# Kernel optimization log

Measured on AMD Instinct MI355X. Metric: run time of the kernel, lower is better.

The kernel has to match this reference:

```python
import jax, jax.numpy as jnp
import numpy as np

WIN = 8          # window_size
DIM = 96         # embedding dim
HEADS = 3        # num_heads
N = WIN * WIN    # tokens per window
B_ = 8192        # total windows (2 images * 64*64 windows)
NUM_WIN = 4096   # windows per image (mask leading dim)


def _relative_position_index():
    # Same construction as the torch module (meshgrid default 'ij').
    ch = np.arange(WIN)
    coords = np.stack(np.meshgrid(ch, ch, indexing="ij"))          # [2, W, W]
    flat = coords.reshape(2, -1)                                     # [2, N]
    rel = flat[:, :, None] - flat[:, None, :]                        # [2, N, N]
    rel = rel.transpose(1, 2, 0).astype(np.int32)                    # [N, N, 2]
    rel[:, :, 0] += WIN - 1
    rel[:, :, 1] += WIN - 1
    rel[:, :, 0] *= 2 * WIN - 1
    return rel.sum(-1)                                               # [N, N] int32


def setup_inputs() -> dict:
    key = jax.random.key(0)
    ks = jax.random.split(key, 8)
    x = jax.random.normal(ks[0], (B_, N, DIM), dtype=jnp.float32)
    mask = jax.random.normal(ks[1], (NUM_WIN, N, N), dtype=jnp.float32)
    s = 0.02
    qkv_w = jax.random.normal(ks[2], (3 * DIM, DIM), dtype=jnp.float32) * s
    qkv_b = jax.random.normal(ks[3], (3 * DIM,), dtype=jnp.float32) * s
    proj_w = jax.random.normal(ks[4], (DIM, DIM), dtype=jnp.float32) * s
    proj_b = jax.random.normal(ks[5], (DIM,), dtype=jnp.float32) * s
    n_bias = (2 * WIN - 1) * (2 * WIN - 1)  # 225
    bias_table = jax.random.normal(ks[6], (n_bias, HEADS), dtype=jnp.float32) * s
    rel_idx = jnp.asarray(_relative_position_index())  # [N, N] int32
    return {"x": x, "mask": mask, "qkv_w": qkv_w, "qkv_b": qkv_b,
            "proj_w": proj_w, "proj_b": proj_b, "bias_table": bias_table,
            "rel_idx": rel_idx}


def reference(x, mask, qkv_w, qkv_b, proj_w, proj_b, bias_table, rel_idx):
    Bw, n, C = x.shape
    hd = C // HEADS
    scale = hd ** (-0.5)
    qkv = (x @ qkv_w.T + qkv_b).reshape(Bw, n, 3, HEADS, hd)
    qkv = jnp.transpose(qkv, (2, 0, 3, 1, 4))
    q, k, v = qkv[0], qkv[1], qkv[2]
    attn = jnp.einsum("bhqd,bhkd->bhqk", q * scale, k)              # [Bw, H, n, n]
    # relative position bias gather: [n, n, H] -> [H, n, n]
    bias = bias_table[rel_idx.reshape(-1)].reshape(n, n, HEADS)
    attn = attn + jnp.transpose(bias, (2, 0, 1))[None]
    # shift mask: broadcast over (batch, heads)
    nw = mask.shape[0]
    attn = attn.reshape(Bw // nw, nw, HEADS, n, n) + mask[None, :, None]
    attn = attn.reshape(Bw, HEADS, n, n)
    attn = jax.nn.softmax(attn, axis=-1)
    out = jnp.einsum("bhqk,bhkd->bhqd", attn, v)                    # [Bw, H, n, hd]
    out = jnp.transpose(out, (0, 2, 1, 3)).reshape(Bw, n, C)
    return out @ proj_w.T + proj_b
```

## Files before the change

kernel.cpp:

```cpp
#include <hip/hip_runtime.h>

typedef __attribute__((ext_vector_type(8))) short short8v;
typedef __attribute__((ext_vector_type(4))) float f32x4;

#define INVLN2 1.4426950408889634f

__device__ __forceinline__ ushort f2bf(float f) {
  union { float f; unsigned int u; } c; c.f = f;
  return (ushort)((c.u + 0x7FFFu + ((c.u >> 16) & 1u)) >> 16);
}

__device__ __forceinline__ unsigned cvtpk(float a, float b) {
  unsigned r;
  asm("v_cvt_pk_bf16_f32 %0, %1, %2" : "=v"(r) : "v"(a), "v"(b));
  return r;
}

__device__ __forceinline__ float exp2w(float x) {
#if __has_builtin(__builtin_amdgcn_exp2f)
  return __builtin_amdgcn_exp2f(x);
#else
  return __expf(x * 0.6931471805599453f);
#endif
}

__device__ __forceinline__ short8v bits8(unsigned a, unsigned b, unsigned c, unsigned d) {
  union { unsigned u[4]; short8v s; } cv;
  cv.u[0] = a; cv.u[1] = b; cv.u[2] = c; cv.u[3] = d;
  return cv.s;
}

__global__ __launch_bounds__(256) void setup_k(
    const float* __restrict__ qkv_w, const float* __restrict__ proj_w,
    const float* __restrict__ bias_table, const int* __restrict__ rel_idx,
    const float* __restrict__ qkv_b,
    ushort* __restrict__ qkv_wb, ushort* __restrict__ proj_wb,
    float* __restrict__ bias_comb, float* __restrict__ qkv_bs) {
  const float qs = 0.17677669529663687f * INVLN2;
  int idx = blockIdx.x * 256 + threadIdx.x;
  if (idx < 27648) {
    qkv_wb[idx] = f2bf(qkv_w[idx] * (idx < 9216 ? qs : 1.0f));
  } else if (idx < 36864) {
    int i = idx - 27648;
    int cw = i / 96, j = i % 96;
    int h = j >> 5, kk = j & 31;
    int g = kk >> 3, b = (kk & 4) >> 2, d = kk & 3;
    int src = h * 32 + 16 * b + 4 * g + d;
    proj_wb[i] = f2bf(proj_w[cw * 96 + src]);
  } else if (idx < 49152) {
    int i = idx - 36864;
    int h = i / 4096, rc = i % 4096;
    bias_comb[i] = bias_table[rel_idx[rc] * 3 + h] * INVLN2;
  } else if (idx < 49440) {
    int i = idx - 49152;
    qkv_bs[i] = qkv_b[i] * (i < 96 ? qs : 1.0f);
  }
}

__global__ __launch_bounds__(256, 2) void winattn(
    const float* __restrict__ x, const float* __restrict__ mask,
    const ushort* __restrict__ qkv_wb, const ushort* __restrict__ proj_wb,
    const float* __restrict__ bias_comb, const float* __restrict__ qkv_bs,
    const float* __restrict__ proj_b, float* __restrict__ out) {
  __shared__ ushort klds[2][64][104];
  __shared__ ushort vts[2][96][64];

  const int bb = blockIdx.x;
  const int t = threadIdx.x;
  const int w = t >> 6;
  const int lane = t & 63;
  const int l15 = lane & 15;
  const int g = lane >> 4;
  const int qrow = w * 16 + l15;

  float4 xr4[2][3][2];
  #pragma unroll
  for (int u = 0; u < 2; ++u) {
    const float* xr = x + ((size_t)(bb + u * 4096) * 64 + qrow) * 96 + g * 8;
    #pragma unroll
    for (int ks3 = 0; ks3 < 3; ++ks3) {
      xr4[u][ks3][0] = *reinterpret_cast<const float4*>(xr + ks3 * 32);
      xr4[u][ks3][1] = *reinterpret_cast<const float4*>(xr + ks3 * 32 + 4);
    }
  }
  const float* mrow = mask + (size_t)bb * 4096 + qrow * 64;
  float4 mk4[4];
  #pragma unroll
  for (int tj = 0; tj < 4; ++tj)
    mk4[tj] = *reinterpret_cast<const float4*>(mrow + tj * 16 + g * 4);

  short8v xa[2][3];
  #pragma unroll
  for (int u = 0; u < 2; ++u)
    #pragma unroll
    for (int ks3 = 0; ks3 < 3; ++ks3) {
      const float4 a0 = xr4[u][ks3][0], a1 = xr4[u][ks3][1];
      xa[u][ks3] = bits8(cvtpk(a0.x, a0.y), cvtpk(a0.z, a0.w),
                         cvtpk(a1.x, a1.y), cvtpk(a1.z, a1.w));
    }

  unsigned qpk[2][6][2];
  short8v bfA[3];
  float4 qbA = {0.f, 0.f, 0.f, 0.f}, qbB;
  float vbA = 0.f, vbB;
  {
    const ushort* wr = qkv_wb + l15 * 96 + g * 8;
    bfA[0] = *reinterpret_cast<const short8v*>(wr);
    bfA[1] = *reinterpret_cast<const short8v*>(wr + 32);
    bfA[2] = *reinterpret_cast<const short8v*>(wr + 64);
    qbA = *reinterpret_cast<const float4*>(qkv_bs + g * 4);
  }
  #pragma unroll
  for (int nt = 0; nt < 18; ++nt) {
    short8v bfB[3];
    if (nt < 17) {
      const ushort* wr = qkv_wb + ((nt + 1) * 16 + l15) * 96 + g * 8;
      bfB[0] = *reinterpret_cast<const short8v*>(wr);
      bfB[1] = *reinterpret_cast<const short8v*>(wr + 32);
      bfB[2] = *reinterpret_cast<const short8v*>(wr + 64);
      if (nt + 1 < 12) qbB = *reinterpret_cast<const float4*>(qkv_bs + (nt + 1) * 16 + g * 4);
      else             vbB = qkv_bs[(nt + 1) * 16 + l15];
    }
    if (nt < 6) {
      #pragma unroll
      for (int u = 0; u < 2; ++u) {
        f32x4 acc = {0.f, 0.f, 0.f, 0.f};
        #pragma unroll
        for (int ks3 = 0; ks3 < 3; ++ks3)
          acc = __builtin_amdgcn_mfma_f32_16x16x32_bf16(bfA[ks3], xa[u][ks3], acc, 0, 0, 0);
        qpk[u][nt][0] = cvtpk(acc[0] + qbA.x, acc[1] + qbA.y);
        qpk[u][nt][1] = cvtpk(acc[2] + qbA.z, acc[3] + qbA.w);
      }
    } else if (nt < 12) {
      const int m = nt - 6;
      const int kcol = 32 * (m >> 1) + 8 * g + 4 * (m & 1);
      #pragma unroll
      for (int u = 0; u < 2; ++u) {
        f32x4 acc = {0.f, 0.f, 0.f, 0.f};
        #pragma unroll
        for (int ks3 = 0; ks3 < 3; ++ks3)
          acc = __builtin_amdgcn_mfma_f32_16x16x32_bf16(bfA[ks3], xa[u][ks3], acc, 0, 0, 0);
        uint2 pk = make_uint2(cvtpk(acc[0] + qbA.x, acc[1] + qbA.y),
                              cvtpk(acc[2] + qbA.z, acc[3] + qbA.w));
        *reinterpret_cast<uint2*>(&klds[u][qrow][kcol]) = pk;
      }
    } else {
      const int vc = nt * 16 + l15 - 192;
      const int tk = (32 * (w >> 1) + 8 * g + 4 * (w & 1)) ^ ((vc & 7) << 3);
      #pragma unroll
      for (int u = 0; u < 2; ++u) {
        f32x4 acc = {0.f, 0.f, 0.f, 0.f};
        #pragma unroll
        for (int ks3 = 0; ks3 < 3; ++ks3)
          acc = __builtin_amdgcn_mfma_f32_16x16x32_bf16(xa[u][ks3], bfA[ks3], acc, 0, 0, 0);
        uint2 pk = make_uint2(cvtpk(acc[0] + vbA, acc[1] + vbA),
                              cvtpk(acc[2] + vbA, acc[3] + vbA));
        *reinterpret_cast<uint2*>(&vts[u][vc][tk]) = pk;
      }
    }
    if (nt < 17) {
      bfA[0] = bfB[0]; bfA[1] = bfB[1]; bfA[2] = bfB[2];
      qbA = qbB; vbA = vbB;
    }
  }

  short8v qf[2][3];
  #pragma unroll
  for (int u = 0; u < 2; ++u)
    #pragma unroll
    for (int h = 0; h < 3; ++h)
      qf[u][h] = bits8(qpk[u][2 * h][0], qpk[u][2 * h][1],
                       qpk[u][2 * h + 1][0], qpk[u][2 * h + 1][1]);

  const float* bcb0 = bias_comb + qrow * 64;
  float4 bc4[3][4];
  #pragma unroll
  for (int h = 0; h < 3; ++h)
    #pragma unroll
    for (int tj = 0; tj < 4; ++tj)
      bc4[h][tj] = *reinterpret_cast<const float4*>(bcb0 + h * 4096 + tj * 16 + g * 4);
  float bmk[3][4][4];
  #pragma unroll
  for (int h = 0; h < 3; ++h)
    #pragma unroll
    for (int tj = 0; tj < 4; ++tj) {
      bmk[h][tj][0] = bc4[h][tj].x + mk4[tj].x * INVLN2;
      bmk[h][tj][1] = bc4[h][tj].y + mk4[tj].y * INVLN2;
      bmk[h][tj][2] = bc4[h][tj].z + mk4[tj].z * INVLN2;
      bmk[h][tj][3] = bc4[h][tj].w + mk4[tj].w * INVLN2;
    }

  __syncthreads();

  short8v ofv[3][2];

  #pragma unroll
  for (int h = 0; h < 3; ++h) {
    f32x4 s[2][4];
    #pragma unroll
    for (int tj = 0; tj < 4; ++tj) {
      #pragma unroll
      for (int u = 0; u < 2; ++u) {
        short8v kf = *reinterpret_cast<const short8v*>(&klds[u][tj * 16 + l15][h * 32 + g * 8]);
        f32x4 z = {0.f, 0.f, 0.f, 0.f};
        s[u][tj] = __builtin_amdgcn_mfma_f32_16x16x32_bf16(kf, qf[u][h], z, 0, 0, 0);
      }
    }
    #pragma unroll
    for (int tj = 0; tj < 4; ++tj)
      #pragma unroll
      for (int u = 0; u < 2; ++u)
        #pragma unroll
        for (int r = 0; r < 4; ++r) s[u][tj][r] += bmk[h][tj][r];
    float inv[2];
    #pragma unroll
    for (int u = 0; u < 2; ++u) {
      #pragma unroll
      for (int tj = 0; tj < 4; ++tj)
        #pragma unroll
        for (int r = 0; r < 4; ++r) s[u][tj][r] = exp2w(s[u][tj][r]);
      float sm = ((s[u][0][0] + s[u][0][1]) + (s[u][0][2] + s[u][0][3]))
               + ((s[u][1][0] + s[u][1][1]) + (s[u][1][2] + s[u][1][3]))
               + ((s[u][2][0] + s[u][2][1]) + (s[u][2][2] + s[u][2][3]))
               + ((s[u][3][0] + s[u][3][1]) + (s[u][3][2] + s[u][3][3]));
      sm += __shfl_xor(sm, 16);
      sm += __shfl_xor(sm, 32);
      inv[u] = __builtin_amdgcn_rcpf(sm);
    }
    unsigned ppk[2][4][2];
    #pragma unroll
    for (int u = 0; u < 2; ++u)
      #pragma unroll
      for (int tj = 0; tj < 4; ++tj) {
        ppk[u][tj][0] = cvtpk(s[u][tj][0], s[u][tj][1]);
        ppk[u][tj][1] = cvtpk(s[u][tj][2], s[u][tj][3]);
      }
    short8v pfv[2][2];
    #pragma unroll
    for (int u = 0; u < 2; ++u)
      #pragma unroll
      for (int ks2 = 0; ks2 < 2; ++ks2)
        pfv[u][ks2] = bits8(ppk[u][2 * ks2][0], ppk[u][2 * ks2][1],
                            ppk[u][2 * ks2 + 1][0], ppk[u][2 * ks2 + 1][1]);
    f32x4 oacc[2][2];
    #pragma unroll
    for (int u = 0; u < 2; ++u)
      #pragma unroll
      for (int nt = 0; nt < 2; ++nt) {
        const int vc = h * 32 + nt * 16 + l15;
        f32x4 o = {0.f, 0.f, 0.f, 0.f};
        #pragma unroll
        for (int ks2 = 0; ks2 < 2; ++ks2) {
          const int tk = (ks2 * 32 + g * 8) ^ ((vc & 7) << 3);
          short8v vf = *reinterpret_cast<const short8v*>(&vts[u][vc][tk]);
          o = __builtin_amdgcn_mfma_f32_16x16x32_bf16(vf, pfv[u][ks2], o, 0, 0, 0);
        }
        oacc[u][nt] = o;
      }
    #pragma unroll
    for (int u = 0; u < 2; ++u) {
      unsigned o00 = cvtpk(oacc[u][0][0] * inv[u], oacc[u][0][1] * inv[u]);
      unsigned o01 = cvtpk(oacc[u][0][2] * inv[u], oacc[u][0][3] * inv[u]);
      unsigned o10 = cvtpk(oacc[u][1][0] * inv[u], oacc[u][1][1] * inv[u]);
      unsigned o11 = cvtpk(oacc[u][1][2] * inv[u], oacc[u][1][3] * inv[u]);
      ofv[h][u] = bits8(o00, o01, o10, o11);
    }
  }

  f32x4 pacc[2][6];
  #pragma unroll
  for (int u = 0; u < 2; ++u)
    #pragma unroll
    for (int nt2 = 0; nt2 < 6; ++nt2) pacc[u][nt2] = (f32x4){0.f, 0.f, 0.f, 0.f};
  #pragma unroll
  for (int h = 0; h < 3; ++h) {
    #pragma unroll
    for (int nt2 = 0; nt2 < 6; ++nt2) {
      short8v pfw = *reinterpret_cast<const short8v*>(proj_wb + (nt2 * 16 + l15) * 96 + h * 32 + g * 8);
      #pragma unroll
      for (int u = 0; u < 2; ++u)
        pacc[u][nt2] = __builtin_amdgcn_mfma_f32_16x16x32_bf16(ofv[h][u], pfw, pacc[u][nt2], 0, 0, 0);
    }
  }

  float pb[6];
  #pragma unroll
  for (int nt2 = 0; nt2 < 6; ++nt2) pb[nt2] = proj_b[nt2 * 16 + l15];
  #pragma unroll
  for (int u = 0; u < 2; ++u) {
    float* ob = out + (size_t)(bb + u * 4096) * 6144 + (w * 16 + g * 4) * 96 + l15;
    #pragma unroll
    for (int nt2 = 0; nt2 < 6; ++nt2)
      #pragma unroll
      for (int r = 0; r < 4; ++r)
        ob[r * 96 + nt2 * 16] = pacc[u][nt2][r] + pb[nt2];
  }
}

extern "C" void kernel_launch(void* const* d_in, const int* in_sizes, int n_in,
                              void* d_out, int out_size, void* d_ws, size_t ws_size,
                              hipStream_t stream) {
  const float* x          = (const float*)d_in[0];
  const float* mask       = (const float*)d_in[1];
  const float* qkv_w      = (const float*)d_in[2];
  const float* qkv_b      = (const float*)d_in[3];
  const float* proj_w     = (const float*)d_in[4];
  const float* proj_b     = (const float*)d_in[5];
  const float* bias_table = (const float*)d_in[6];
  const int*   rel_idx    = (const int*)d_in[7];

  char* ws = (char*)d_ws;
  ushort* qkv_wb    = (ushort*)ws;
  ushort* proj_wb   = (ushort*)(ws + 55296);
  float*  bias_comb = (float*)(ws + 55296 + 18432);
  float*  qkv_bs    = (float*)(ws + 55296 + 18432 + 49152);

  setup_k<<<194, 256, 0, stream>>>(qkv_w, proj_w, bias_table, rel_idx, qkv_b,
                                   qkv_wb, proj_wb, bias_comb, qkv_bs);
  winattn<<<4096, 256, 0, stream>>>(x, mask, qkv_wb, proj_wb,
                                    bias_comb, qkv_bs, proj_b, (float*)d_out);
}
```

Baseline: 165.1 us.

## Process four windows per block to amortize weight and bias loads

```diff
diff --git a/kernel.cpp b/kernel.cpp
--- a/kernel.cpp
+++ b/kernel.cpp
@@ -57,13 +57,13 @@
   }
 }
 
-__global__ __launch_bounds__(256, 2) void winattn(
+__global__ __launch_bounds__(256, 1) void winattn(
     const float* __restrict__ x, const float* __restrict__ mask,
     const ushort* __restrict__ qkv_wb, const ushort* __restrict__ proj_wb,
     const float* __restrict__ bias_comb, const float* __restrict__ qkv_bs,
     const float* __restrict__ proj_b, float* __restrict__ out) {
-  __shared__ ushort klds[2][64][104];
-  __shared__ ushort vts[2][96][64];
+  __shared__ ushort klds[4][64][104];
+  __shared__ ushort vts[4][96][64];
 
   const int bb = blockIdx.x;
   const int t = threadIdx.x;
@@ -73,25 +73,30 @@
   const int g = lane >> 4;
   const int qrow = w * 16 + l15;
 
-  float4 xr4[2][3][2];
-  #pragma unroll
-  for (int u = 0; u < 2; ++u) {
-    const float* xr = x + ((size_t)(bb + u * 4096) * 64 + qrow) * 96 + g * 8;
+
+  float4 xr4[4][3][2];
+  #pragma unroll
+  for (int u = 0; u < 4; ++u) {
+    const int win = bb + ((u >> 1) << 11) + ((u & 1) << 12);
+    const float* xr = x + ((size_t)win * 64 + qrow) * 96 + g * 8;
     #pragma unroll
     for (int ks3 = 0; ks3 < 3; ++ks3) {
       xr4[u][ks3][0] = *reinterpret_cast<const float4*>(xr + ks3 * 32);
       xr4[u][ks3][1] = *reinterpret_cast<const float4*>(xr + ks3 * 32 + 4);
     }
   }
-  const float* mrow = mask + (size_t)bb * 4096 + qrow * 64;
-  float4 mk4[4];
-  #pragma unroll
-  for (int tj = 0; tj < 4; ++tj)
-    mk4[tj] = *reinterpret_cast<const float4*>(mrow + tj * 16 + g * 4);
-
-  short8v xa[2][3];
-  #pragma unroll
-  for (int u = 0; u < 2; ++u)
+  float4 mk4[2][4];
+  #pragma unroll
+  for (int p = 0; p < 2; ++p) {
+    const float* mrow = mask + (size_t)(bb + (p << 11)) * 4096 + qrow * 64;
+    #pragma unroll
+    for (int tj = 0; tj < 4; ++tj)
+      mk4[p][tj] = *reinterpret_cast<const float4*>(mrow + tj * 16 + g * 4);
+  }
+
+  short8v xa[4][3];
+  #pragma unroll
+  for (int u = 0; u < 4; ++u)
     #pragma unroll
     for (int ks3 = 0; ks3 < 3; ++ks3) {
       const float4 a0 = xr4[u][ks3][0], a1 = xr4[u][ks3][1];
@@ -99,7 +104,7 @@
                          cvtpk(a1.x, a1.y), cvtpk(a1.z, a1.w));
     }
 
-  unsigned qpk[2][6][2];
+  unsigned qpk[4][6][2];
   short8v bfA[3];
   float4 qbA = {0.f, 0.f, 0.f, 0.f}, qbB;
   float vbA = 0.f, vbB;
@@ -123,7 +128,7 @@
     }
     if (nt < 6) {
       #pragma unroll
-      for (int u = 0; u < 2; ++u) {
+      for (int u = 0; u < 4; ++u) {
         f32x4 acc = {0.f, 0.f, 0.f, 0.f};
         #pragma unroll
         for (int ks3 = 0; ks3 < 3; ++ks3)
@@ -135,7 +140,7 @@
       const int m = nt - 6;
       const int kcol = 32 * (m >> 1) + 8 * g + 4 * (m & 1);
       #pragma unroll
-      for (int u = 0; u < 2; ++u) {
+      for (int u = 0; u < 4; ++u) {
         f32x4 acc = {0.f, 0.f, 0.f, 0.f};
         #pragma unroll
         for (int ks3 = 0; ks3 < 3; ++ks3)
@@ -148,7 +153,7 @@
       const int vc = nt * 16 + l15 - 192;
       const int tk = (32 * (w >> 1) + 8 * g + 4 * (w & 1)) ^ ((vc & 7) << 3);
       #pragma unroll
-      for (int u = 0; u < 2; ++u) {
+      for (int u = 0; u < 4; ++u) {
         f32x4 acc = {0.f, 0.f, 0.f, 0.f};
         #pragma unroll
         for (int ks3 = 0; ks3 < 3; ++ks3)
@@ -164,43 +169,46 @@
     }
   }
 
-  short8v qf[2][3];
-  #pragma unroll
-  for (int u = 0; u < 2; ++u)
+  short8v qf[4][3];
+  #pragma unroll
+  for (int u = 0; u < 4; ++u)
     #pragma unroll
     for (int h = 0; h < 3; ++h)
       qf[u][h] = bits8(qpk[u][2 * h][0], qpk[u][2 * h][1],
                        qpk[u][2 * h + 1][0], qpk[u][2 * h + 1][1]);
 
   const float* bcb0 = bias_comb + qrow * 64;
-  float4 bc4[3][4];
+  float bcf[3][4][4];
   #pragma unroll
   for (int h = 0; h < 3; ++h)
     #pragma unroll
-    for (int tj = 0; tj < 4; ++tj)
-      bc4[h][tj] = *reinterpret_cast<const float4*>(bcb0 + h * 4096 + tj * 16 + g * 4);
-  float bmk[3][4][4];
-  #pragma unroll
-  for (int h = 0; h < 3; ++h)
-    #pragma unroll
     for (int tj = 0; tj < 4; ++tj) {
-      bmk[h][tj][0] = bc4[h][tj].x + mk4[tj].x * INVLN2;
-      bmk[h][tj][1] = bc4[h][tj].y + mk4[tj].y * INVLN2;
-      bmk[h][tj][2] = bc4[h][tj].z + mk4[tj].z * INVLN2;
-      bmk[h][tj][3] = bc4[h][tj].w + mk4[tj].w * INVLN2;
+      float4 b4 = *reinterpret_cast<const float4*>(bcb0 + h * 4096 + tj * 16 + g * 4);
+      bcf[h][tj][0] = b4.x; bcf[h][tj][1] = b4.y;
+      bcf[h][tj][2] = b4.z; bcf[h][tj][3] = b4.w;
+    }
+  float mkp[2][4][4];
+  #pragma unroll
+  for (int p = 0; p < 2; ++p)
+    #pragma unroll
+    for (int tj = 0; tj < 4; ++tj) {
+      mkp[p][tj][0] = mk4[p][tj].x * INVLN2;
+      mkp[p][tj][1] = mk4[p][tj].y * INVLN2;
+      mkp[p][tj][2] = mk4[p][tj].z * INVLN2;
+      mkp[p][tj][3] = mk4[p][tj].w * INVLN2;
     }
 
   __syncthreads();
 
-  short8v ofv[3][2];
+  short8v ofv[3][4];
 
   #pragma unroll
   for (int h = 0; h < 3; ++h) {
-    f32x4 s[2][4];
+    f32x4 s[4][4];
     #pragma unroll
     for (int tj = 0; tj < 4; ++tj) {
       #pragma unroll
-      for (int u = 0; u < 2; ++u) {
+      for (int u = 0; u < 4; ++u) {
         short8v kf = *reinterpret_cast<const short8v*>(&klds[u][tj * 16 + l15][h * 32 + g * 8]);
         f32x4 z = {0.f, 0.f, 0.f, 0.f};
         s[u][tj] = __builtin_amdgcn_mfma_f32_16x16x32_bf16(kf, qf[u][h], z, 0, 0, 0);
@@ -209,12 +217,15 @@
     #pragma unroll
     for (int tj = 0; tj < 4; ++tj)
       #pragma unroll
-      for (int u = 0; u < 2; ++u)
-        #pragma unroll
-        for (int r = 0; r < 4; ++r) s[u][tj][r] += bmk[h][tj][r];
-    float inv[2];
-    #pragma unroll
-    for (int u = 0; u < 2; ++u) {
+      for (int r = 0; r < 4; ++r) {
+        const float b0 = bcf[h][tj][r] + mkp[0][tj][r];
+        const float b1 = bcf[h][tj][r] + mkp[1][tj][r];
+        s[0][tj][r] += b0; s[1][tj][r] += b0;
+        s[2][tj][r] += b1; s[3][tj][r] += b1;
+      }
+    float inv[4];
+    #pragma unroll
+    for (int u = 0; u < 4; ++u) {
       #pragma unroll
       for (int tj = 0; tj < 4; ++tj)
         #pragma unroll
@@ -227,24 +238,23 @@
       sm += __shfl_xor(sm, 32);
       inv[u] = __builtin_amdgcn_rcpf(sm);
     }
-    unsigned ppk[2][4][2];
-    #pragma unroll
-    for (int u = 0; u < 2; ++u)
-      #pragma unroll
-      for (int tj = 0; tj < 4; ++tj) {
-        ppk[u][tj][0] = cvtpk(s[u][tj][0], s[u][tj][1]);
-        ppk[u][tj][1] = cvtpk(s[u][tj][2], s[u][tj][3]);
-      }
-    short8v pfv[2][2];
-    #pragma unroll
-    for (int u = 0; u < 2; ++u)
-      #pragma unroll
-      for (int ks2 = 0; ks2 < 2; ++ks2)
-        pfv[u][ks2] = bits8(ppk[u][2 * ks2][0], ppk[u][2 * ks2][1],
-                            ppk[u][2 * ks2 + 1][0], ppk[u][2 * ks2 + 1][1]);
-    f32x4 oacc[2][2];
-    #pragma unroll
-    for (int u = 0; u < 2; ++u)
+    short8v pfv[4][2];
+    #pragma unroll
+    for (int u = 0; u < 4; ++u) {
+      unsigned p00 = cvtpk(s[u][0][0], s[u][0][1]);
+      unsigned p01 = cvtpk(s[u][0][2], s[u][0][3]);
+      unsigned p10 = cvtpk(s[u][1][0], s[u][1][1]);
+      unsigned p11 = cvtpk(s[u][1][2], s[u][1][3]);
+      unsigned p20 = cvtpk(s[u][2][0], s[u][2][1]);
+      unsigned p21 = cvtpk(s[u][2][2], s[u][2][3]);
+      unsigned p30 = cvtpk(s[u][3][0], s[u][3][1]);
+      unsigned p31 = cvtpk(s[u][3][2], s[u][3][3]);
+      pfv[u][0] = bits8(p00, p01, p10, p11);
+      pfv[u][1] = bits8(p20, p21, p30, p31);
+    }
+    #pragma unroll
+    for (int u = 0; u < 4; ++u) {
+      f32x4 oacc[2];
       #pragma unroll
       for (int nt = 0; nt < 2; ++nt) {
         const int vc = h * 32 + nt * 16 + l15;
@@ -255,21 +265,19 @@
           short8v vf = *reinterpret_cast<const short8v*>(&vts[u][vc][tk]);
           o = __builtin_amdgcn_mfma_f32_16x16x32_bf16(vf, pfv[u][ks2], o, 0, 0, 0);
         }
-        oacc[u][nt] = o;
-      }
-    #pragma unroll
-    for (int u = 0; u < 2; ++u) {
-      unsigned o00 = cvtpk(oacc[u][0][0] * inv[u], oacc[u][0][1] * inv[u]);
-      unsigned o01 = cvtpk(oacc[u][0][2] * inv[u], oacc[u][0][3] * inv[u]);
-      unsigned o10 = cvtpk(oacc[u][1][0] * inv[u], oacc[u][1][1] * inv[u]);
-      unsigned o11 = cvtpk(oacc[u][1][2] * inv[u], oacc[u][1][3] * inv[u]);
+        oacc[nt] = o;
+      }
+      unsigned o00 = cvtpk(oacc[0][0] * inv[u], oacc[0][1] * inv[u]);
+      unsigned o01 = cvtpk(oacc[0][2] * inv[u], oacc[0][3] * inv[u]);
+      unsigned o10 = cvtpk(oacc[1][0] * inv[u], oacc[1][1] * inv[u]);
+      unsigned o11 = cvtpk(oacc[1][2] * inv[u], oacc[1][3] * inv[u]);
       ofv[h][u] = bits8(o00, o01, o10, o11);
     }
   }
 
-  f32x4 pacc[2][6];
-  #pragma unroll
-  for (int u = 0; u < 2; ++u)
+  f32x4 pacc[4][6];
+  #pragma unroll
+  for (int u = 0; u < 4; ++u)
     #pragma unroll
     for (int nt2 = 0; nt2 < 6; ++nt2) pacc[u][nt2] = (f32x4){0.f, 0.f, 0.f, 0.f};
   #pragma unroll
@@ -278,7 +286,7 @@
     for (int nt2 = 0; nt2 < 6; ++nt2) {
       short8v pfw = *reinterpret_cast<const short8v*>(proj_wb + (nt2 * 16 + l15) * 96 + h * 32 + g * 8);
       #pragma unroll
-      for (int u = 0; u < 2; ++u)
+      for (int u = 0; u < 4; ++u)
         pacc[u][nt2] = __builtin_amdgcn_mfma_f32_16x16x32_bf16(ofv[h][u], pfw, pacc[u][nt2], 0, 0, 0);
     }
   }
@@ -287,8 +295,9 @@
   #pragma unroll
   for (int nt2 = 0; nt2 < 6; ++nt2) pb[nt2] = proj_b[nt2 * 16 + l15];
   #pragma unroll
-  for (int u = 0; u < 2; ++u) {
-    float* ob = out + (size_t)(bb + u * 4096) * 6144 + (w * 16 + g * 4) * 96 + l15;
+  for (int u = 0; u < 4; ++u) {
+    const int win = bb + ((u >> 1) << 11) + ((u & 1) << 12);
+    float* ob = out + (size_t)win * 6144 + (w * 16 + g * 4) * 96 + l15;
     #pragma unroll
     for (int nt2 = 0; nt2 < 6; ++nt2)
       #pragma unroll
@@ -317,6 +326,6 @@
 
   setup_k<<<194, 256, 0, stream>>>(qkv_w, proj_w, bias_table, rel_idx, qkv_b,
                                    qkv_wb, proj_wb, bias_comb, qkv_bs);
-  winattn<<<4096, 256, 0, stream>>>(x, mask, qkv_wb, proj_wb,
+  winattn<<<2048, 256, 0, stream>>>(x, mask, qkv_wb, proj_wb,
                                     bias_comb, qkv_bs, proj_b, (float*)d_out);
 }
```

Result: no change. 162.2 us (-1.7%).
